# Performance work log

Hardware: AMD Instinct MI355X
Metric: run time of the kernel (lower is better)

## Reference

```python
import jax, jax.numpy as jnp
import numpy as np

B, D, E, K = 8192, 1024, 8, 2048  # tokens, dim, num_experts, k (per-expert capacity)


def setup_inputs() -> dict:
    key = jax.random.key(0)
    ks = jax.random.split(key, 5)
    x = jax.random.normal(ks[0], (B, D), dtype=jnp.float32)
    Wr = jax.random.normal(ks[1], (D, E), dtype=jnp.float32) * 0.02
    br = jnp.zeros((E,), jnp.float32)
    W1 = jax.random.normal(ks[2], (E, D, 4 * D), dtype=jnp.float32) * 0.02
    b1 = jnp.zeros((E, 4 * D), jnp.float32)
    W2 = jax.random.normal(ks[3], (E, 4 * D, D), dtype=jnp.float32) * 0.02
    b2 = jnp.zeros((E, D), jnp.float32)
    return {"x": x, "Wr": Wr, "br": br, "W1": W1, "b1": b1, "W2": W2, "b2": b2}


def _dispatch_weights(x, Wr, br):
    # Expert-choice routing: softmax over experts per token, each expert picks top-K tokens.
    gate = jax.nn.softmax(x @ Wr + br, axis=-1)          # [B, E]
    vals, idx = jax.lax.top_k(gate.T, K)                 # [E, K] each
    w = jnp.zeros((x.shape[0], E), x.dtype)
    w = w.at[idx.reshape(-1), jnp.repeat(jnp.arange(E), K)].set(vals.reshape(-1))
    # torch source builds dispatch_weights via .tolist(), detaching it from autograd
    return jax.lax.stop_gradient(w)                      # [B, E]


def reference(x, Wr, br, W1, b1, W2, b2):
    w = _dispatch_weights(x, Wr, br)                     # [B, E]
    mask = (w > 0).astype(x.dtype)                       # [B, E]
    xm = x[None, :, :] * mask.T[:, :, None]              # [E, B, D] (dense masked input, as in source)
    h = jax.nn.relu(jnp.einsum('ebd,edh->ebh', xm, W1) + b1[:, None, :])   # [E, B, 4D]
    y = jnp.einsum('ebh,ehd->ebd', h, W2) + b2[:, None, :]                 # [E, B, D]
    out = jnp.einsum('ebd,be->bd', y, w)                 # weighted combine over experts
    return out
```

## Files before the change

kernel.cpp:

```cpp
#include <hip/hip_runtime.h>
#include <hip/hip_bf16.h>

#define BTOK 8192
#define DDIM 1024
#define NEXP 8
#define KCAP 2048
#define HDIM 4096
#define MB ((size_t)1048576)

typedef __attribute__((ext_vector_type(4))) float f32x4;
typedef __attribute__((ext_vector_type(8))) short bf16x8;

__device__ __forceinline__ unsigned short f2bf(float f) {
    union { float f; unsigned u; } v; v.f = f;
    unsigned r = v.u + 0x7fffu + ((v.u >> 16) & 1u);
    return (unsigned short)(r >> 16);
}

typedef __attribute__((address_space(3))) unsigned int lds_u32;
typedef __attribute__((address_space(1))) const unsigned int glb_u32;
__device__ __forceinline__ void gl_lds16(const void* g, void* l) {
    __builtin_amdgcn_global_load_lds((glb_u32*)g, (lds_u32*)l, 16, 0, 0);
}

__global__ __launch_bounds__(256) void router_kernel(
    const float* __restrict__ x, const float* __restrict__ Wr,
    const float* __restrict__ br, float* __restrict__ gateT,
    unsigned short* __restrict__ xb) {
    __shared__ float wr_s[NEXP][DDIM];
    int t = threadIdx.x;
    for (int i = t; i < NEXP * DDIM; i += 256) {
        int e = i >> 10, d = i & 1023;
        wr_s[e][d] = Wr[d * NEXP + e];
    }
    __syncthreads();
    int wid = t >> 6, lane = t & 63;
    int b = blockIdx.x * 4 + wid;
    const float4* xr = (const float4*)(x + (size_t)b * DDIM);
    float4 xv[4];
#pragma unroll
    for (int j = 0; j < 4; j++) xv[j] = xr[j * 64 + lane];
#pragma unroll
    for (int j = 0; j < 4; j++) {
        short4 s;
        s.x = (short)f2bf(xv[j].x); s.y = (short)f2bf(xv[j].y);
        s.z = (short)f2bf(xv[j].z); s.w = (short)f2bf(xv[j].w);
        *(short4*)(xb + (size_t)b * DDIM + (j * 64 + lane) * 4) = s;
    }
    double acc[NEXP];
#pragma unroll
    for (int e = 0; e < NEXP; e++) {
        double a = 0.0;
#pragma unroll
        for (int j = 0; j < 4; j++) {
            float4 wv = ((const float4*)&wr_s[e][0])[j * 64 + lane];
            a += (double)xv[j].x * wv.x + (double)xv[j].y * wv.y
               + (double)xv[j].z * wv.z + (double)xv[j].w * wv.w;
        }
#pragma unroll
        for (int s = 1; s < 64; s <<= 1) a += __shfl_xor(a, s, 64);
        acc[e] = a + (double)br[e];
    }
    if (lane == 0) {
        double mx = acc[0];
#pragma unroll
        for (int e = 1; e < NEXP; e++) mx = fmax(mx, acc[e]);
        double p[NEXP]; double ssum = 0.0;
#pragma unroll
        for (int e = 0; e < NEXP; e++) { p[e] = exp(acc[e] - mx); ssum += p[e]; }
        double inv = 1.0 / ssum;
#pragma unroll
        for (int e = 0; e < NEXP; e++) gateT[e * BTOK + b] = (float)(p[e] * inv);
    }
}

__global__ __launch_bounds__(256) void select_kernel(
    const float* __restrict__ gateT, unsigned* __restrict__ meta) {
    int e = blockIdx.x, t = threadIdx.x;
    const float* g = gateT + e * BTOK;
    __shared__ unsigned hist[256];
    __shared__ unsigned sh_prefix;
    __shared__ int sh_rem;
    if (t == 0) { sh_prefix = 0; sh_rem = KCAP; }
    __syncthreads();
    for (int pass = 0; pass < 4; pass++) {
        int shift = 24 - pass * 8;
        hist[t] = 0;
        __syncthreads();
        unsigned pfx = sh_prefix;
        for (int i = t; i < BTOK; i += 256) {
            unsigned key = __float_as_uint(g[i]);
            if (pass == 0 || (key >> (shift + 8)) == pfx)
                atomicAdd(&hist[(key >> shift) & 255u], 1u);
        }
        __syncthreads();
        if (t == 0) {
            int rem = sh_rem, cum = 0, d = 0;
            for (int dd = 255; dd >= 0; dd--) {
                cum += (int)hist[dd];
                if (cum >= rem) { d = dd; break; }
            }
            sh_rem = rem - (cum - (int)hist[d]);
            sh_prefix = (pfx << 8) | (unsigned)d;
        }
        __syncthreads();
    }
    unsigned cutoff = sh_prefix;
    int cnt = 0;
    for (int i = t; i < BTOK; i += 256)
        if (__float_as_uint(g[i]) > cutoff) cnt++;
    __shared__ int red[256];
    red[t] = cnt; __syncthreads();
    for (int s = 128; s > 0; s >>= 1) { if (t < s) red[t] += red[t + s]; __syncthreads(); }
    if (t == 0) { meta[e] = cutoff; meta[NEXP + e] = (unsigned)red[0]; }
}

__global__ __launch_bounds__(256) void build_kernel(
    const float* __restrict__ gateT, const unsigned* __restrict__ meta,
    unsigned* __restrict__ cnt, int* __restrict__ idx_list, float* __restrict__ wt_list) {
    int e = blockIdx.y;
    int b = blockIdx.x * 256 + threadIdx.x;
    float gv = gateT[(size_t)e * BTOK + b];
    if (__float_as_uint(gv) > meta[e]) {
        unsigned pos = atomicAdd(&cnt[e], 1u);
        if (pos < KCAP) {
            idx_list[(size_t)e * KCAP + pos] = b;
            wt_list[(size_t)e * KCAP + pos] = gv;
        }
    }
}

__global__ __launch_bounds__(256) void tie_kernel(
    const float* __restrict__ gateT, const unsigned* __restrict__ meta,
    unsigned* __restrict__ cnt, int* __restrict__ idx_list, float* __restrict__ wt_list) {
    int e = blockIdx.x, t = threadIdx.x;
    unsigned cutoff = meta[e];
    int need = KCAP - (int)meta[NEXP + e];
    const float* g = gateT + (size_t)e * BTOK;
    __shared__ int pre[256];
    int base = t * 32;
    int c = 0;
    for (int j = 0; j < 32; j++) c += (__float_as_uint(g[base + j]) == cutoff) ? 1 : 0;
    pre[t] = c;
    __syncthreads();
    for (int s = 1; s < 256; s <<= 1) {
        int v = (t >= s) ? pre[t - s] : 0;
        __syncthreads();
        pre[t] += v;
        __syncthreads();
    }
    int rank = pre[t] - c;
    for (int j = 0; j < 32; j++) {
        float gv = g[base + j];
        if (__float_as_uint(gv) == cutoff) {
            if (rank < need) {
                unsigned pos = atomicAdd(&cnt[e], 1u);
                if (pos < KCAP) {
                    idx_list[(size_t)e * KCAP + pos] = base + j;
                    wt_list[(size_t)e * KCAP + pos] = gv;
                }
            }
            rank++;
        }
    }
}

__global__ __launch_bounds__(256) void invb_kernel(
    const int* __restrict__ idx_list, int* __restrict__ inv) {
    int i = blockIdx.x * 256 + threadIdx.x;
    int e = i >> 11, slot = i & (KCAP - 1);
    inv[(size_t)e * BTOK + idx_list[i]] = slot;
}

__global__ __launch_bounds__(256) void tcvt_kernel(
    const float* __restrict__ src, unsigned short* __restrict__ dst, int R, int C) {
    size_t zoff = (size_t)blockIdx.z * R * C;
    src += zoff; dst += zoff;
    __shared__ unsigned short tile[64][72];
    int c0 = blockIdx.x * 64, r0 = blockIdx.y * 64;
    int t = threadIdx.x;
    int cq = t & 15, rr = t >> 4;
#pragma unroll
    for (int ri = 0; ri < 4; ri++) {
        int r = ri * 16 + rr;
        float4 v = *(const float4*)(src + (size_t)(r0 + r) * C + c0 + cq * 4);
        tile[cq * 4 + 0][r] = f2bf(v.x);
        tile[cq * 4 + 1][r] = f2bf(v.y);
        tile[cq * 4 + 2][r] = f2bf(v.z);
        tile[cq * 4 + 3][r] = f2bf(v.w);
    }
    __syncthreads();
    int rq = t & 15, cc = t >> 4;
#pragma unroll
    for (int ci = 0; ci < 4; ci++) {
        int c = ci * 16 + cc;
        *(short4*)(dst + (size_t)(c0 + c) * R + r0 + rq * 4) = *(const short4*)&tile[c][rq * 4];
    }
}


#define ASLOT 4096
#define BSLOT 8192

__global__ __launch_bounds__(512, 4) void gemm1_kernel(
    const unsigned short* __restrict__ xb, const unsigned short* __restrict__ w1t,
    const float* __restrict__ b1, const int* __restrict__ idx_list,
    unsigned short* __restrict__ h) {
    int bid = blockIdx.x;
    int e = bid & 7, idx = bid >> 3;
    int m0 = (idx & 15) * 128, n0 = (idx >> 4) * 256;
    w1t      += (size_t)e * DDIM * HDIM;
    b1       += (size_t)e * HDIM;
    idx_list += (size_t)e * KCAP;
    h        += (size_t)e * KCAP * HDIM;
    __shared__ unsigned short As[3 * ASLOT];
    __shared__ unsigned short Bs[3 * BSLOT];
    __shared__ int toks[128];
    int t = threadIdx.x;
    if (t < 128) toks[t] = idx_list[m0 + t];
    __syncthreads();
    int w = t >> 6, lane = t & 63, l4 = lane >> 2;
    unsigned swz = (unsigned)(((lane & 3) ^ ((lane >> 3) & 3)) << 4);
    const char* pa  = (const char*)(xb + (size_t)toks[w * 16 + l4] * DDIM) + swz;
    const char* pb0 = (const char*)(w1t + (size_t)(n0 + w * 16 + l4) * DDIM) + swz;
    const char* pb1 = (const char*)(w1t + (size_t)(n0 + 128 + w * 16 + l4) * DDIM) + swz;
    unsigned short* da  = As + (w * 16) * 32;
    unsigned short* db0 = Bs + (w * 16) * 32;
    unsigned short* db1 = Bs + (128 + w * 16) * 32;
#define ST1(slot, koff) do {                                         \
    gl_lds16(pa  + (koff), da  + (slot) * ASLOT);                    \
    gl_lds16(pb0 + (koff), db0 + (slot) * BSLOT);                    \
    gl_lds16(pb1 + (koff), db1 + (slot) * BSLOT); } while (0)
    int wm = w >> 2, wn = w & 3;
    int fr = lane & 15, kg = lane >> 4;
    unsigned koffr = (unsigned)((kg ^ ((fr >> 1) & 3)) << 4);
    const int NT = DDIM / 32;
    f32x4 acc[4][4] = {};
    ST1(0, 0); ST1(1, 64);
    asm volatile("s_waitcnt vmcnt(3)" ::: "memory");
    __builtin_amdgcn_s_barrier();
    size_t ko = 128;
    int sw = 2, sr = 0;
    for (int kt = 0; kt < NT; kt++) {
        if (kt + 2 < NT) { ST1(sw, ko); ko += 64; }
        const char* ab = (const char*)As + sr * (ASLOT * 2);
        const char* bb = (const char*)Bs + sr * (BSLOT * 2);
        bf16x8 af[4], bf[4];
#pragma unroll
        for (int mf = 0; mf < 4; mf++)
            af[mf] = *(const bf16x8*)(ab + (wm * 64 + mf * 16 + fr) * 64 + koffr);
#pragma unroll
        for (int nf = 0; nf < 4; nf++)
            bf[nf] = *(const bf16x8*)(bb + (wn * 64 + nf * 16 + fr) * 64 + koffr);
        __builtin_amdgcn_s_setprio(1);
#pragma unroll
        for (int mf = 0; mf < 4; mf++)
#pragma unroll
            for (int nf = 0; nf < 4; nf++)
                acc[mf][nf] = __builtin_amdgcn_mfma_f32_16x16x32_bf16(
                    af[mf], bf[nf], acc[mf][nf], 0, 0, 0);
        __builtin_amdgcn_s_setprio(0);
        if (kt + 1 < NT) {
            if (kt + 2 < NT) asm volatile("s_waitcnt vmcnt(3)" ::: "memory");
            else             asm volatile("s_waitcnt vmcnt(0)" ::: "memory");
            __builtin_amdgcn_s_barrier();
        }
        sw = (sw == 2) ? 0 : sw + 1;
        sr = (sr == 2) ? 0 : sr + 1;
    }
#undef ST1
    int hi = lane >> 4;
#pragma unroll
    for (int nf = 0; nf < 4; nf++) {
        int col = n0 + wn * 64 + nf * 16 + fr;
        float bias = b1[col];
#pragma unroll
        for (int mf = 0; mf < 4; mf++) {
            int r0 = wm * 64 + mf * 16 + hi * 4;
#pragma unroll
            for (int r = 0; r < 4; r++) {
                float v = fmaxf(acc[mf][nf][r] + bias, 0.f);
                h[(size_t)(m0 + r0 + r) * HDIM + col] = f2bf(v);
            }
        }
    }
}

__global__ __launch_bounds__(512, 4) void gemm2y_kernel(
    const unsigned short* __restrict__ h, const unsigned short* __restrict__ w2t,
    const float* __restrict__ b2, const float* __restrict__ wt_list,
    float* __restrict__ yb) {
    int bid = blockIdx.x;
    int e = bid & 7, idx = bid >> 3;
    int m0 = (idx & 15) * 128, n0 = (idx >> 4) * 256;
    h       += (size_t)e * KCAP * HDIM;
    w2t     += (size_t)e * DDIM * HDIM;
    b2      += (size_t)e * DDIM;
    wt_list += (size_t)e * KCAP;
    yb      += (size_t)e * KCAP * DDIM;
    __shared__ unsigned short As[3 * ASLOT];
    __shared__ unsigned short Bs[3 * BSLOT];
    __shared__ float wts[128];
    int t = threadIdx.x;
    if (t < 128) wts[t] = wt_list[m0 + t];
    __syncthreads();
    int w = t >> 6, lane = t & 63, l4 = lane >> 2;
    unsigned swz = (unsigned)(((lane & 3) ^ ((lane >> 3) & 3)) << 4);
    const char* pa  = (const char*)(h + (size_t)(m0 + w * 16 + l4) * HDIM) + swz;
    const char* pb0 = (const char*)(w2t + (size_t)(n0 + w * 16 + l4) * HDIM) + swz;
    const char* pb1 = (const char*)(w2t + (size_t)(n0 + 128 + w * 16 + l4) * HDIM) + swz;
    unsigned short* da  = As + (w * 16) * 32;
    unsigned short* db0 = Bs + (w * 16) * 32;
    unsigned short* db1 = Bs + (128 + w * 16) * 32;
#define ST2(slot, koff) do {                                         \
    gl_lds16(pa  + (koff), da  + (slot) * ASLOT);                    \
    gl_lds16(pb0 + (koff), db0 + (slot) * BSLOT);                    \
    gl_lds16(pb1 + (koff), db1 + (slot) * BSLOT); } while (0)
    int wm = w >> 2, wn = w & 3;
    int fr = lane & 15, kg = lane >> 4;
    unsigned koffr = (unsigned)((kg ^ ((fr >> 1) & 3)) << 4);
    const int NT = HDIM / 32;
    f32x4 acc[4][4] = {};
    ST2(0, 0); ST2(1, 64);
    asm volatile("s_waitcnt vmcnt(3)" ::: "memory");
    __builtin_amdgcn_s_barrier();
    size_t ko = 128;
    int sw = 2, sr = 0;
    for (int kt = 0; kt < NT; kt++) {
        if (kt + 2 < NT) { ST2(sw, ko); ko += 64; }
        const char* ab = (const char*)As + sr * (ASLOT * 2);
        const char* bb = (const char*)Bs + sr * (BSLOT * 2);
        bf16x8 af[4], bf[4];
#pragma unroll
        for (int mf = 0; mf < 4; mf++)
            af[mf] = *(const bf16x8*)(ab + (wm * 64 + mf * 16 + fr) * 64 + koffr);
#pragma unroll
        for (int nf = 0; nf < 4; nf++)
            bf[nf] = *(const bf16x8*)(bb + (wn * 64 + nf * 16 + fr) * 64 + koffr);
        __builtin_amdgcn_s_setprio(1);
#pragma unroll
        for (int mf = 0; mf < 4; mf++)
#pragma unroll
            for (int nf = 0; nf < 4; nf++)
                acc[mf][nf] = __builtin_amdgcn_mfma_f32_16x16x32_bf16(
                    af[mf], bf[nf], acc[mf][nf], 0, 0, 0);
        __builtin_amdgcn_s_setprio(0);
        if (kt + 1 < NT) {
            if (kt + 2 < NT) asm volatile("s_waitcnt vmcnt(3)" ::: "memory");
            else             asm volatile("s_waitcnt vmcnt(0)" ::: "memory");
            __builtin_amdgcn_s_barrier();
        }
        sw = (sw == 2) ? 0 : sw + 1;
        sr = (sr == 2) ? 0 : sr + 1;
    }
#undef ST2
    int hi = lane >> 4;
#pragma unroll
    for (int nf = 0; nf < 4; nf++) {
        int col = n0 + wn * 64 + nf * 16 + fr;
        float bias = b2[col];
#pragma unroll
        for (int mf = 0; mf < 4; mf++) {
            int r0 = wm * 64 + mf * 16 + hi * 4;
#pragma unroll
            for (int r = 0; r < 4; r++) {
                int lrow = r0 + r;
                yb[(size_t)(m0 + lrow) * DDIM + col] = wts[lrow] * (acc[mf][nf][r] + bias);
            }
        }
    }
}

__global__ __launch_bounds__(256) void combine_kernel(
    const float* __restrict__ yb, const int* __restrict__ inv,
    float* __restrict__ out) {
    int b = blockIdx.x, t = threadIdx.x;
    float4 acc = {0.f, 0.f, 0.f, 0.f};
#pragma unroll
    for (int e = 0; e < NEXP; e++) {
        int s = inv[(size_t)e * BTOK + b];
        if (s >= 0) {
            float4 v = *(const float4*)(yb + ((size_t)e * KCAP + s) * DDIM + t * 4);
            acc.x += v.x; acc.y += v.y; acc.z += v.z; acc.w += v.w;
        }
    }
    *(float4*)(out + (size_t)b * DDIM + t * 4) = acc;
}

extern "C" void kernel_launch(void* const* d_in, const int* in_sizes, int n_in,
                              void* d_out, int out_size, void* d_ws, size_t ws_size,
                              hipStream_t stream) {
    const float* x  = (const float*)d_in[0];
    const float* Wr = (const float*)d_in[1];
    const float* br = (const float*)d_in[2];
    const float* W1 = (const float*)d_in[3];
    const float* b1 = (const float*)d_in[4];
    const float* W2 = (const float*)d_in[5];
    const float* b2 = (const float*)d_in[6];
    float* out = (float*)d_out;

    char* ws = (char*)d_ws;
    float*    gateT    = (float*)ws;
    unsigned* meta     = (unsigned*)(ws + 262144);
    unsigned* cnt      = meta + 16;
    int*      idx_list = (int*)(ws + 327680);
    float*    wt_list  = (float*)(ws + 393216);
    int*      inv      = (int*)(ws + 458752);
    unsigned short* xbuf = (unsigned short*)(ws + 1 * MB);
    unsigned short* w1t  = (unsigned short*)(ws + 17 * MB);
    unsigned short* w2t  = (unsigned short*)(ws + 81 * MB);
    unsigned short* hbuf = (unsigned short*)(ws + 145 * MB);
    float*          yb   = (float*)(ws + 273 * MB);
    const size_t NEED = 337 * MB;
    if (ws_size < NEED) return;

    hipMemsetAsync(cnt, 0, NEXP * sizeof(unsigned), stream);
    hipMemsetAsync(inv, 0xFF, (size_t)NEXP * BTOK * sizeof(int), stream);

    router_kernel<<<dim3(BTOK / 4), 256, 0, stream>>>(x, Wr, br, gateT, xbuf);
    select_kernel<<<dim3(NEXP), 256, 0, stream>>>(gateT, meta);
    build_kernel<<<dim3(BTOK / 256, NEXP), 256, 0, stream>>>(gateT, meta, cnt, idx_list, wt_list);
    tie_kernel<<<dim3(NEXP), 256, 0, stream>>>(gateT, meta, cnt, idx_list, wt_list);

    tcvt_kernel<<<dim3(HDIM / 64, DDIM / 64, NEXP), 256, 0, stream>>>(W1, w1t, DDIM, HDIM);
    tcvt_kernel<<<dim3(DDIM / 64, HDIM / 64, NEXP), 256, 0, stream>>>(W2, w2t, HDIM, DDIM);
    invb_kernel<<<dim3(NEXP * KCAP / 256), 256, 0, stream>>>(idx_list, inv);

    gemm1_kernel<<<dim3((KCAP / 128) * (HDIM / 256) * NEXP), 512, 0, stream>>>(
        xbuf, w1t, b1, idx_list, hbuf);
    gemm2y_kernel<<<dim3((KCAP / 128) * (DDIM / 256) * NEXP), 512, 0, stream>>>(
        hbuf, w2t, b2, wt_list, yb);
    combine_kernel<<<dim3(BTOK), 256, 0, stream>>>(yb, inv, out);
}
```

Baseline: 567.5 us.

## Use 4-wave blocks with 128x64 per-wave MFMA tiles in expert GEMMs

Both expert GEMM kernels change from 8 waves of 512 threads, each computing a 64x64 sub-tile, to 4 waves of 256 threads, each computing a 128x64 sub-tile (8x4 MFMA fragments). The block tile stays 128x256, so each thread now issues six global-to-LDS loads per stage instead of three, and the vmcnt waits are adjusted to match. The aim is more MFMA work per LDS fragment read and fewer waves contending at barriers. In exchange, per-thread register use for accumulators doubles and occupancy drops, which leaves less latency hiding.

```diff
diff --git a/kernel.cpp b/kernel.cpp
--- a/kernel.cpp
+++ b/kernel.cpp
@@ -202,7 +202,7 @@
 #define ASLOT 4096
 #define BSLOT 8192
 
-__global__ __launch_bounds__(512, 4) void gemm1_kernel(
+__global__ __launch_bounds__(256, 2) void gemm1_kernel(
     const unsigned short* __restrict__ xb, const unsigned short* __restrict__ w1t,
     const float* __restrict__ b1, const int* __restrict__ idx_list,
     unsigned short* __restrict__ h) {
@@ -219,25 +219,31 @@
     int t = threadIdx.x;
     if (t < 128) toks[t] = idx_list[m0 + t];
     __syncthreads();
-    int w = t >> 6, lane = t & 63, l4 = lane >> 2;
-    unsigned swz = (unsigned)(((lane & 3) ^ ((lane >> 3) & 3)) << 4);
-    const char* pa  = (const char*)(xb + (size_t)toks[w * 16 + l4] * DDIM) + swz;
-    const char* pb0 = (const char*)(w1t + (size_t)(n0 + w * 16 + l4) * DDIM) + swz;
-    const char* pb1 = (const char*)(w1t + (size_t)(n0 + 128 + w * 16 + l4) * DDIM) + swz;
-    unsigned short* da  = As + (w * 16) * 32;
-    unsigned short* db0 = Bs + (w * 16) * 32;
-    unsigned short* db1 = Bs + (128 + w * 16) * 32;
-#define ST1(slot, koff) do {                                         \
-    gl_lds16(pa  + (koff), da  + (slot) * ASLOT);                    \
-    gl_lds16(pb0 + (koff), db0 + (slot) * BSLOT);                    \
-    gl_lds16(pb1 + (koff), db1 + (slot) * BSLOT); } while (0)
-    int wm = w >> 2, wn = w & 3;
+    int w = t >> 6, lane = t & 63;
+    int r1 = t >> 2;
+    unsigned cs = (unsigned)(((t & 3) ^ ((t >> 3) & 3)) << 4);
+    const char* paA  = (const char*)(xb + (size_t)toks[r1] * DDIM) + cs;
+    const char* paA2 = (const char*)(xb + (size_t)toks[r1 + 64] * DDIM) + cs;
+    const char* pbB  = (const char*)(w1t + (size_t)(n0 + r1) * DDIM) + cs;
+    const char* pbB2 = (const char*)(w1t + (size_t)(n0 + 64 + r1) * DDIM) + cs;
+    const char* pbB3 = (const char*)(w1t + (size_t)(n0 + 128 + r1) * DDIM) + cs;
+    const char* pbB4 = (const char*)(w1t + (size_t)(n0 + 192 + r1) * DDIM) + cs;
+    unsigned short* dA = As + (w * 16) * 32;
+    unsigned short* dB = Bs + (w * 16) * 32;
+#define ST1(slot, kb) {                                                  \
+    gl_lds16(paA  + (kb), dA + (slot) * ASLOT);                          \
+    gl_lds16(paA2 + (kb), dA + (slot) * ASLOT + 2048);                   \
+    gl_lds16(pbB  + (kb), dB + (slot) * BSLOT);                          \
+    gl_lds16(pbB2 + (kb), dB + (slot) * BSLOT + 2048);                   \
+    gl_lds16(pbB3 + (kb), dB + (slot) * BSLOT + 4096);                   \
+    gl_lds16(pbB4 + (kb), dB + (slot) * BSLOT + 6144); }
+    int wn = w;
     int fr = lane & 15, kg = lane >> 4;
     unsigned koffr = (unsigned)((kg ^ ((fr >> 1) & 3)) << 4);
     const int NT = DDIM / 32;
-    f32x4 acc[4][4] = {};
+    f32x4 acc[8][4] = {};
     ST1(0, 0); ST1(1, 64);
-    asm volatile("s_waitcnt vmcnt(3)" ::: "memory");
+    asm volatile("s_waitcnt vmcnt(6)" ::: "memory");
     __builtin_amdgcn_s_barrier();
     size_t ko = 128;
     int sw = 2, sr = 0;
@@ -245,23 +251,23 @@
         if (kt + 2 < NT) { ST1(sw, ko); ko += 64; }
         const char* ab = (const char*)As + sr * (ASLOT * 2);
         const char* bb = (const char*)Bs + sr * (BSLOT * 2);
-        bf16x8 af[4], bf[4];
-#pragma unroll
-        for (int mf = 0; mf < 4; mf++)
-            af[mf] = *(const bf16x8*)(ab + (wm * 64 + mf * 16 + fr) * 64 + koffr);
+        bf16x8 af[8], bf[4];
+#pragma unroll
+        for (int mf = 0; mf < 8; mf++)
+            af[mf] = *(const bf16x8*)(ab + (mf * 16 + fr) * 64 + koffr);
 #pragma unroll
         for (int nf = 0; nf < 4; nf++)
             bf[nf] = *(const bf16x8*)(bb + (wn * 64 + nf * 16 + fr) * 64 + koffr);
         __builtin_amdgcn_s_setprio(1);
 #pragma unroll
-        for (int mf = 0; mf < 4; mf++)
+        for (int mf = 0; mf < 8; mf++)
 #pragma unroll
             for (int nf = 0; nf < 4; nf++)
                 acc[mf][nf] = __builtin_amdgcn_mfma_f32_16x16x32_bf16(
                     af[mf], bf[nf], acc[mf][nf], 0, 0, 0);
         __builtin_amdgcn_s_setprio(0);
         if (kt + 1 < NT) {
-            if (kt + 2 < NT) asm volatile("s_waitcnt vmcnt(3)" ::: "memory");
+            if (kt + 2 < NT) asm volatile("s_waitcnt vmcnt(6)" ::: "memory");
             else             asm volatile("s_waitcnt vmcnt(0)" ::: "memory");
             __builtin_amdgcn_s_barrier();
         }
@@ -275,8 +281,8 @@
         int col = n0 + wn * 64 + nf * 16 + fr;
         float bias = b1[col];
 #pragma unroll
-        for (int mf = 0; mf < 4; mf++) {
-            int r0 = wm * 64 + mf * 16 + hi * 4;
+        for (int mf = 0; mf < 8; mf++) {
+            int r0 = mf * 16 + hi * 4;
 #pragma unroll
             for (int r = 0; r < 4; r++) {
                 float v = fmaxf(acc[mf][nf][r] + bias, 0.f);
@@ -286,7 +292,7 @@
     }
 }
 
-__global__ __launch_bounds__(512, 4) void gemm2y_kernel(
+__global__ __launch_bounds__(256, 2) void gemm2y_kernel(
     const unsigned short* __restrict__ h, const unsigned short* __restrict__ w2t,
     const float* __restrict__ b2, const float* __restrict__ wt_list,
     float* __restrict__ yb) {
@@ -304,25 +310,31 @@
     int t = threadIdx.x;
     if (t < 128) wts[t] = wt_list[m0 + t];
     __syncthreads();
-    int w = t >> 6, lane = t & 63, l4 = lane >> 2;
-    unsigned swz = (unsigned)(((lane & 3) ^ ((lane >> 3) & 3)) << 4);
-    const char* pa  = (const char*)(h + (size_t)(m0 + w * 16 + l4) * HDIM) + swz;
-    const char* pb0 = (const char*)(w2t + (size_t)(n0 + w * 16 + l4) * HDIM) + swz;
-    const char* pb1 = (const char*)(w2t + (size_t)(n0 + 128 + w * 16 + l4) * HDIM) + swz;
-    unsigned short* da  = As + (w * 16) * 32;
-    unsigned short* db0 = Bs + (w * 16) * 32;
-    unsigned short* db1 = Bs + (128 + w * 16) * 32;
-#define ST2(slot, koff) do {                                         \
-    gl_lds16(pa  + (koff), da  + (slot) * ASLOT);                    \
-    gl_lds16(pb0 + (koff), db0 + (slot) * BSLOT);                    \
-    gl_lds16(pb1 + (koff), db1 + (slot) * BSLOT); } while (0)
-    int wm = w >> 2, wn = w & 3;
+    int w = t >> 6, lane = t & 63;
+    int r1 = t >> 2;
+    unsigned cs = (unsigned)(((t & 3) ^ ((t >> 3) & 3)) << 4);
+    const char* paA  = (const char*)(h + (size_t)(m0 + r1) * HDIM) + cs;
+    const char* paA2 = (const char*)(h + (size_t)(m0 + 64 + r1) * HDIM) + cs;
+    const char* pbB  = (const char*)(w2t + (size_t)(n0 + r1) * HDIM) + cs;
+    const char* pbB2 = (const char*)(w2t + (size_t)(n0 + 64 + r1) * HDIM) + cs;
+    const char* pbB3 = (const char*)(w2t + (size_t)(n0 + 128 + r1) * HDIM) + cs;
+    const char* pbB4 = (const char*)(w2t + (size_t)(n0 + 192 + r1) * HDIM) + cs;
+    unsigned short* dA = As + (w * 16) * 32;
+    unsigned short* dB = Bs + (w * 16) * 32;
+#define ST2(slot, kb) {                                                  \
+    gl_lds16(paA  + (kb), dA + (slot) * ASLOT);                          \
+    gl_lds16(paA2 + (kb), dA + (slot) * ASLOT + 2048);                   \
+    gl_lds16(pbB  + (kb), dB + (slot) * BSLOT);                          \
+    gl_lds16(pbB2 + (kb), dB + (slot) * BSLOT + 2048);                   \
+    gl_lds16(pbB3 + (kb), dB + (slot) * BSLOT + 4096);                   \
+    gl_lds16(pbB4 + (kb), dB + (slot) * BSLOT + 6144); }
+    int wn = w;
     int fr = lane & 15, kg = lane >> 4;
     unsigned koffr = (unsigned)((kg ^ ((fr >> 1) & 3)) << 4);
     const int NT = HDIM / 32;
-    f32x4 acc[4][4] = {};
+    f32x4 acc[8][4] = {};
     ST2(0, 0); ST2(1, 64);
-    asm volatile("s_waitcnt vmcnt(3)" ::: "memory");
+    asm volatile("s_waitcnt vmcnt(6)" ::: "memory");
     __builtin_amdgcn_s_barrier();
     size_t ko = 128;
     int sw = 2, sr = 0;
@@ -330,23 +342,23 @@
         if (kt + 2 < NT) { ST2(sw, ko); ko += 64; }
         const char* ab = (const char*)As + sr * (ASLOT * 2);
         const char* bb = (const char*)Bs + sr * (BSLOT * 2);
-        bf16x8 af[4], bf[4];
-#pragma unroll
-        for (int mf = 0; mf < 4; mf++)
-            af[mf] = *(const bf16x8*)(ab + (wm * 64 + mf * 16 + fr) * 64 + koffr);
+        bf16x8 af[8], bf[4];
+#pragma unroll
+        for (int mf = 0; mf < 8; mf++)
+            af[mf] = *(const bf16x8*)(ab + (mf * 16 + fr) * 64 + koffr);
 #pragma unroll
         for (int nf = 0; nf < 4; nf++)
             bf[nf] = *(const bf16x8*)(bb + (wn * 64 + nf * 16 + fr) * 64 + koffr);
         __builtin_amdgcn_s_setprio(1);
 #pragma unroll
-        for (int mf = 0; mf < 4; mf++)
+        for (int mf = 0; mf < 8; mf++)
 #pragma unroll
             for (int nf = 0; nf < 4; nf++)
                 acc[mf][nf] = __builtin_amdgcn_mfma_f32_16x16x32_bf16(
                     af[mf], bf[nf], acc[mf][nf], 0, 0, 0);
         __builtin_amdgcn_s_setprio(0);
         if (kt + 1 < NT) {
-            if (kt + 2 < NT) asm volatile("s_waitcnt vmcnt(3)" ::: "memory");
+            if (kt + 2 < NT) asm volatile("s_waitcnt vmcnt(6)" ::: "memory");
             else             asm volatile("s_waitcnt vmcnt(0)" ::: "memory");
             __builtin_amdgcn_s_barrier();
         }
@@ -360,8 +372,8 @@
         int col = n0 + wn * 64 + nf * 16 + fr;
         float bias = b2[col];
 #pragma unroll
-        for (int mf = 0; mf < 4; mf++) {
-            int r0 = wm * 64 + mf * 16 + hi * 4;
+        for (int mf = 0; mf < 8; mf++) {
+            int r0 = mf * 16 + hi * 4;
 #pragma unroll
             for (int r = 0; r < 4; r++) {
                 int lrow = r0 + r;
@@ -426,9 +438,9 @@
     tcvt_kernel<<<dim3(DDIM / 64, HDIM / 64, NEXP), 256, 0, stream>>>(W2, w2t, HDIM, DDIM);
     invb_kernel<<<dim3(NEXP * KCAP / 256), 256, 0, stream>>>(idx_list, inv);
 
-    gemm1_kernel<<<dim3((KCAP / 128) * (HDIM / 256) * NEXP), 512, 0, stream>>>(
+    gemm1_kernel<<<dim3((KCAP / 128) * (HDIM / 256) * NEXP), 256, 0, stream>>>(
         xbuf, w1t, b1, idx_list, hbuf);
-    gemm2y_kernel<<<dim3((KCAP / 128) * (DDIM / 256) * NEXP), 512, 0, stream>>>(
+    gemm2y_kernel<<<dim3((KCAP / 128) * (DDIM / 256) * NEXP), 256, 0, stream>>>(
         hbuf, w2t, b2, wt_list, yb);
     combine_kernel<<<dim3(BTOK), 256, 0, stream>>>(yb, inv, out);
 }
```

Measured after the change: 600.4 us. 5.8% more time.
